# Performance work log

Hardware: AMD Instinct MI355X
Metric: run time of the kernel (lower is better)

## Reference

```python
import jax, jax.numpy as jnp
import numpy as np

N_NODES = 15
EMBED_DIM = 2048
F1 = 1024
F2 = 512
N_EDGES = 120


def gcn_conv(x, src, dst, W, b):
    # PyG GCNConv: h = D^{-1/2} (A + I) D^{-1/2} (x W) + b
    h = x @ W                                   # [N, F_out]
    n = h.shape[0]
    loops = jnp.arange(n)
    s = jnp.concatenate([src, loops])
    d = jnp.concatenate([dst, loops])
    deg = jax.ops.segment_sum(jnp.ones_like(d, dtype=h.dtype), d, num_segments=n)
    dinv = jax.lax.rsqrt(deg)                   # deg >= 1 due to self loops
    norm = dinv[s] * dinv[d]                    # [E+N]
    out = jax.ops.segment_sum(h[s] * norm[:, None], d, num_segments=n)
    return out + b


def attention_pool(x, attW):
    # SimGNN-style attention: global ctx = tanh(mean(x W)); scores = sigmoid(x @ ctx)
    ctx = jnp.tanh(jnp.mean(x @ attW, axis=0))  # [F2]
    scores = jax.nn.sigmoid(x @ ctx)            # [N]
    return x.T @ scores                         # [F2]


def setup_inputs() -> dict:
    key = jax.random.key(0)
    ks = jax.random.split(key, 16)
    d = {}
    d['features_1'] = jax.random.normal(ks[0], (N_NODES,), dtype=jnp.float32)
    d['edge_index_1'] = jax.random.randint(ks[1], (2, N_EDGES), 0, N_NODES, dtype=jnp.int32)
    d['target'] = jax.random.uniform(ks[2], (3,), dtype=jnp.float32)
    def lin(k, fi, fo):
        s = 1.0 / np.sqrt(fi)
        kw, kb = jax.random.split(k)
        return (jax.random.uniform(kw, (fi, fo), minval=-s, maxval=s, dtype=jnp.float32),
                jax.random.uniform(kb, (fo,), minval=-s, maxval=s, dtype=jnp.float32))
    d['W1'], d['b1'] = lin(ks[3], 15, 15 * 32)
    d['W2'], d['b2'] = lin(ks[4], 15 * 32, 15 * 128)
    d['W3'], d['b3'] = lin(ks[5], 15 * 128, 15 * EMBED_DIM)
    d['gW1'], d['gb1'] = lin(ks[6], EMBED_DIM, F1)
    d['gW2'], d['gb2'] = lin(ks[7], F1, F2)
    d['attW'] = jax.random.normal(ks[8], (F2, F2), dtype=jnp.float32) * (1.0 / np.sqrt(F2))
    d['fcW'], d['fcb'] = lin(ks[9], F2, 3)
    return d


def reference(features_1, edge_index_1, target, W1, b1, W2, b2, W3, b3,
              gW1, gb1, gW2, gb2, attW, fcW, fcb):
    # embed MLP: 15 -> 480 -> 1920 -> 15*embed_dim
    h = jax.nn.relu(features_1 @ W1 + b1)
    h = jax.nn.relu(h @ W2 + b2)
    h = (h @ W3 + b3).reshape(N_NODES, EMBED_DIM)
    src, dst = edge_index_1[0], edge_index_1[1]
    x = jax.nn.relu(gcn_conv(h, src, dst, gW1, gb1))
    x = gcn_conv(x, src, dst, gW2, gb2)
    rep = attention_pool(x, attW)               # [F2]
    logits = rep @ fcW + fcb                    # [3]
    cls = jnp.argmax(target)
    loss = -jax.nn.log_softmax(logits)[cls]
    predictions = jax.nn.softmax(logits)
    return loss, predictions
```

## Files before the change

kernel.cpp:

```cpp
#include <hip/hip_runtime.h>
#include <math.h>

#define NN 15
#define EMBED 2048
#define F1D 1024
#define F2D 512
#define NE 120
#define H1_DIM 480
#define H2_DIM 1920
#define H3_DIM 30720

#define OFF_A    0
#define OFF_H2   256
#define OFF_P3   2304
#define OFF_XG1  248064
#define OFF_P1   278784
#define OFF_XG2  524544
#define OFF_P2   539904
#define OFF_X2   662784
#define OFF_XBAR 670464
#define OFF_CTX  670976

__device__ inline void f4ma(float4& a, float s, const float4& w) {
    a.x += s * w.x; a.y += s * w.y; a.z += s * w.z; a.w += s * w.w;
}
__device__ inline void f4acc(float4& a, const float4& b) {
    a.x += b.x; a.y += b.y; a.z += b.z; a.w += b.w;
}

__global__ void k1_h2(const float* __restrict__ f, const float* __restrict__ W1,
                      const float* __restrict__ b1, const float* __restrict__ W2,
                      const float* __restrict__ b2, const int* __restrict__ edges,
                      float* __restrict__ ws) {
    int tid = threadIdx.x;
    if (blockIdx.x == 60) {
        __shared__ float dinv[NN];
        __shared__ float A[NN * NN];
        if (tid < NN) {
            int deg = 1;
            for (int i = 0; i < NE; ++i) deg += (edges[NE + i] == tid) ? 1 : 0;
            dinv[tid] = rsqrtf((float)deg);
        }
        __syncthreads();
        if (tid < NN * NN) {
            int r = tid / NN, c = tid % NN;
            A[tid] = (r == c) ? dinv[r] * dinv[r] : 0.0f;
        }
        __syncthreads();
        if (tid == 0) {
            for (int i = 0; i < NE; ++i) {
                int s = edges[i], d = edges[NE + i];
                A[d * NN + s] += dinv[s] * dinv[d];
            }
        }
        __syncthreads();
        if (tid < NN * NN) ws[OFF_A + tid] = A[tid];
        return;
    }
    __shared__ float h1[H1_DIM];
    __shared__ float4 red[32][8];
    float fr[NN];
#pragma unroll
    for (int k = 0; k < NN; ++k) fr[k] = f[k];
    for (int j = tid; j < H1_DIM; j += 256) {
        float acc = b1[j];
#pragma unroll
        for (int k = 0; k < NN; ++k) acc += fr[k] * W1[k * H1_DIM + j];
        h1[j] = fmaxf(acc, 0.0f);
    }
    __syncthreads();
    int jg = tid & 7, kc = tid >> 3;
    int j = blockIdx.x * 32 + jg * 4;
    float4 acc = make_float4(0.f, 0.f, 0.f, 0.f);
    for (int r = 0; r < 15; ++r) {
        int k = kc * 15 + r;
        float4 w = *(const float4*)(W2 + k * H2_DIM + j);
        f4ma(acc, h1[k], w);
    }
    red[kc][jg] = acc;
    __syncthreads();
    for (int s = 16; s >= 1; s >>= 1) {
        if (kc < s) f4acc(red[kc][jg], red[kc + s][jg]);
        __syncthreads();
    }
    if (kc == 0) {
        float4 b = *(const float4*)(b2 + j);
        float4 v = red[0][jg];
        v.x = fmaxf(v.x + b.x, 0.f); v.y = fmaxf(v.y + b.y, 0.f);
        v.z = fmaxf(v.z + b.z, 0.f); v.w = fmaxf(v.w + b.w, 0.f);
        *(float4*)(ws + OFF_H2 + j) = v;
    }
}

__global__ void k2_h3(const float* __restrict__ W3, float* __restrict__ ws) {
    __shared__ float h2l[240];
    __shared__ float4 red[128];
    int tid = threadIdx.x;
    int cb = blockIdx.x, kc = blockIdx.y;
    int kbase = kc * 240;
    for (int i = tid; i < 240; i += 256) h2l[i] = ws[OFF_H2 + kbase + i];
    __syncthreads();
    int f4i = tid & 127, rg = tid >> 7;
    int col = cb * 512 + f4i * 4;
    float4 acc = make_float4(0.f, 0.f, 0.f, 0.f);
    const float* wp = W3 + (size_t)(kbase + rg) * H3_DIM + col;
#pragma unroll 8
    for (int i = 0; i < 120; ++i) {
        float4 w = *(const float4*)wp;
        f4ma(acc, h2l[2 * i + rg], w);
        wp += 2 * (size_t)H3_DIM;
    }
    if (rg == 1) red[f4i] = acc;
    __syncthreads();
    if (rg == 0) {
        f4acc(acc, red[f4i]);
        *(float4*)(ws + OFF_P3 + (size_t)kc * H3_DIM + col) = acc;
    }
}

__global__ void k3_agg1(const float* __restrict__ b3, float* __restrict__ ws) {
    __shared__ float Al[NN * NN];
    __shared__ float S[NN][32];
    int tid = threadIdx.x;
    int c0 = blockIdx.x * 32;
    for (int i = tid; i < NN * NN; i += 256) Al[i] = ws[OFF_A + i];
    for (int q = tid; q < NN * 32; q += 256) {
        int m = q >> 5, c = q & 31;
        int j = m * EMBED + c0 + c;
        float s = b3[j];
#pragma unroll
        for (int p = 0; p < 8; ++p) s += ws[OFF_P3 + p * H3_DIM + j];
        S[m][c] = s;
    }
    __syncthreads();
    for (int q = tid; q < NN * 32; q += 256) {
        int n = q >> 5, c = q & 31;
        float x = 0.f;
#pragma unroll
        for (int m = 0; m < NN; ++m) x += Al[n * NN + m] * S[m][c];
        ws[OFF_XG1 + n * EMBED + c0 + c] = x;
    }
}

template<int IN, int OUT, int ECH>
__global__ void k_mmP(const float* __restrict__ X, const float* __restrict__ W,
                      float* __restrict__ P) {
    __shared__ float Xl[NN * ECH];
    __shared__ float4 red[8][32][NN];
    int tid = threadIdx.x;
    int e0 = blockIdx.y * ECH;
    for (int i = tid; i < NN * ECH; i += 256) {
        int n = i / ECH, e = i - n * ECH;
        Xl[i] = X[n * IN + e0 + e];
    }
    __syncthreads();
    int fg = tid & 31, kt = tid >> 5;
    int f = blockIdx.x * 128 + fg * 4;
    float4 acc[NN];
#pragma unroll
    for (int n = 0; n < NN; ++n) acc[n] = make_float4(0.f, 0.f, 0.f, 0.f);
    const int RPT = ECH / 8;
    for (int r = 0; r < RPT; ++r) {
        int e = kt * RPT + r;
        float4 w = *(const float4*)(W + (size_t)(e0 + e) * OUT + f);
#pragma unroll
        for (int n = 0; n < NN; ++n) f4ma(acc[n], Xl[n * ECH + e], w);
    }
    __syncthreads();
#pragma unroll
    for (int n = 0; n < NN; ++n) red[kt][fg][n] = acc[n];
    __syncthreads();
    for (int s = 4; s >= 1; s >>= 1) {
        if (kt < s) {
#pragma unroll
            for (int n = 0; n < NN; ++n) f4acc(red[kt][fg][n], red[kt + s][fg][n]);
        }
        __syncthreads();
    }
    if (kt == 0) {
#pragma unroll
        for (int n = 0; n < NN; ++n) {
            float4 v = red[0][fg][n];
            *(float4*)(P + (size_t)blockIdx.y * NN * OUT + n * OUT + f) = v;
        }
    }
}

__global__ void k5_fin1(const float* __restrict__ gb1, float* __restrict__ ws) {
    __shared__ float Al[NN * NN];
    __shared__ float S[NN][64];
    int tid = threadIdx.x;
    int f0 = blockIdx.x * 64;
    for (int i = tid; i < NN * NN; i += 256) Al[i] = ws[OFF_A + i];
    for (int q = tid; q < NN * 64; q += 256) {
        int n = q >> 6, c = q & 63;
        float s = gb1[f0 + c];
#pragma unroll
        for (int p = 0; p < 16; ++p) s += ws[OFF_P1 + p * (NN * F1D) + n * F1D + f0 + c];
        S[n][c] = fmaxf(s, 0.f);
    }
    __syncthreads();
    for (int q = tid; q < NN * 64; q += 256) {
        int n = q >> 6, c = q & 63;
        float x = 0.f;
#pragma unroll
        for (int m = 0; m < NN; ++m) x += Al[n * NN + m] * S[m][c];
        ws[OFF_XG2 + n * F1D + f0 + c] = x;
    }
}

__global__ void k7_fin2(const float* __restrict__ gb2, float* __restrict__ ws) {
    __shared__ float S[NN][64];
    int tid = threadIdx.x;
    int f0 = blockIdx.x * 64;
    for (int q = tid; q < NN * 64; q += 256) {
        int n = q >> 6, c = q & 63;
        float s = gb2[f0 + c];
#pragma unroll
        for (int p = 0; p < 16; ++p) s += ws[OFF_P2 + p * (NN * F2D) + n * F2D + f0 + c];
        S[n][c] = s;
        ws[OFF_X2 + n * F2D + f0 + c] = s;
    }
    __syncthreads();
    if (tid < 64) {
        float s = 0.f;
#pragma unroll
        for (int n = 0; n < NN; ++n) s += S[n][tid];
        ws[OFF_XBAR + f0 + tid] = s * (1.0f / 15.0f);
    }
}

__global__ void k8_ctx(const float* __restrict__ attW, float* __restrict__ ws) {
    __shared__ float xb[F2D];
    __shared__ float4 red[64][4];
    int tid = threadIdx.x;
    for (int e = tid; e < F2D; e += 256) xb[e] = ws[OFF_XBAR + e];
    __syncthreads();
    int fg = tid & 3, kt = tid >> 2;
    int f = blockIdx.x * 16 + fg * 4;
    float4 acc = make_float4(0.f, 0.f, 0.f, 0.f);
    for (int r = 0; r < 8; ++r) {
        int e = kt * 8 + r;
        float4 w = *(const float4*)(attW + e * F2D + f);
        f4ma(acc, xb[e], w);
    }
    red[kt][fg] = acc;
    __syncthreads();
    for (int s = 32; s >= 1; s >>= 1) {
        if (kt < s) f4acc(red[kt][fg], red[kt + s][fg]);
        __syncthreads();
    }
    if (kt == 0) {
        float4 v = red[0][fg];
        ws[OFF_CTX + f + 0] = tanhf(v.x);
        ws[OFF_CTX + f + 1] = tanhf(v.y);
        ws[OFF_CTX + f + 2] = tanhf(v.z);
        ws[OFF_CTX + f + 3] = tanhf(v.w);
    }
}

__global__ void k9_final(const float* __restrict__ fcW, const float* __restrict__ fcb,
                         const float* __restrict__ target, const float* __restrict__ ws,
                         float* __restrict__ out) {
    __shared__ float x2l[NN * F2D];
    __shared__ float ctxl[F2D];
    __shared__ float scores[16];
    __shared__ float rep[F2D];
    __shared__ float logits[3];
    int tid = threadIdx.x;
    for (int i = tid; i < NN * F2D; i += 256) x2l[i] = ws[OFF_X2 + i];
    for (int i = tid; i < F2D; i += 256) ctxl[i] = ws[OFF_CTX + i];
    __syncthreads();
    {
        int g = tid >> 4, l = tid & 15;
        if (g < NN) {
            float p = 0.f;
            for (int i = 0; i < 32; ++i) {
                int e = l + 16 * i;
                p += x2l[g * F2D + e] * ctxl[e];
            }
            p += __shfl_xor(p, 1); p += __shfl_xor(p, 2);
            p += __shfl_xor(p, 4); p += __shfl_xor(p, 8);
            if (l == 0) scores[g] = 1.0f / (1.0f + expf(-p));
        }
    }
    __syncthreads();
    for (int fi = tid; fi < F2D; fi += 256) {
        float v = 0.f;
#pragma unroll
        for (int n = 0; n < NN; ++n) v += x2l[n * F2D + fi] * scores[n];
        rep[fi] = v;
    }
    __syncthreads();
    if (tid < 192) {
        int j = tid >> 6, l = tid & 63;
        float p = 0.f;
        for (int i = 0; i < 8; ++i) {
            int e = l + 64 * i;
            p += rep[e] * fcW[e * 3 + j];
        }
        p += __shfl_xor(p, 1); p += __shfl_xor(p, 2); p += __shfl_xor(p, 4);
        p += __shfl_xor(p, 8); p += __shfl_xor(p, 16); p += __shfl_xor(p, 32);
        if (l == 0) logits[j] = p + fcb[j];
    }
    __syncthreads();
    if (tid == 0) {
        float t0 = target[0], t1 = target[1], t2 = target[2];
        int cls = 0; float best = t0;
        if (t1 > best) { best = t1; cls = 1; }
        if (t2 > best) { cls = 2; }
        float l0 = logits[0], l1 = logits[1], l2 = logits[2];
        float m = fmaxf(l0, fmaxf(l1, l2));
        float e0 = expf(l0 - m), e1 = expf(l1 - m), e2 = expf(l2 - m);
        float s = e0 + e1 + e2;
        float lc = (cls == 0) ? l0 : ((cls == 1) ? l1 : l2);
        out[0] = -(lc - m - logf(s));
        out[1] = e0 / s; out[2] = e1 / s; out[3] = e2 / s;
    }
}

extern "C" void kernel_launch(void* const* d_in, const int* in_sizes, int n_in,
                              void* d_out, int out_size, void* d_ws, size_t ws_size,
                              hipStream_t stream) {
    const float* f    = (const float*)d_in[0];
    const int*   ei   = (const int*)d_in[1];
    const float* tgt  = (const float*)d_in[2];
    const float* W1   = (const float*)d_in[3];
    const float* b1   = (const float*)d_in[4];
    const float* W2   = (const float*)d_in[5];
    const float* b2   = (const float*)d_in[6];
    const float* W3   = (const float*)d_in[7];
    const float* b3   = (const float*)d_in[8];
    const float* gW1  = (const float*)d_in[9];
    const float* gb1  = (const float*)d_in[10];
    const float* gW2  = (const float*)d_in[11];
    const float* gb2  = (const float*)d_in[12];
    const float* attW = (const float*)d_in[13];
    const float* fcW  = (const float*)d_in[14];
    const float* fcb  = (const float*)d_in[15];
    float* ws  = (float*)d_ws;
    float* out = (float*)d_out;

    k1_h2<<<dim3(61), dim3(256), 0, stream>>>(f, W1, b1, W2, b2, ei, ws);
    k2_h3<<<dim3(60, 8), dim3(256), 0, stream>>>(W3, ws);
    k3_agg1<<<dim3(64), dim3(256), 0, stream>>>(b3, ws);
    k_mmP<2048, 1024, 128><<<dim3(8, 16), dim3(256), 0, stream>>>(ws + OFF_XG1, gW1, ws + OFF_P1);
    k5_fin1<<<dim3(16), dim3(256), 0, stream>>>(gb1, ws);
    k_mmP<1024, 512, 64><<<dim3(4, 16), dim3(256), 0, stream>>>(ws + OFF_XG2, gW2, ws + OFF_P2);
    k7_fin2<<<dim3(8), dim3(256), 0, stream>>>(gb2, ws);
    k8_ctx<<<dim3(32), dim3(256), 0, stream>>>(attW, ws);
    k9_final<<<dim3(1), dim3(256), 0, stream>>>(fcW, fcb, tgt, ws, out);
}
```

Before: 414.2 us.

## Skip zero ReLU activations in W3 GEMV and reshape k2 grid

The h2 x W3 GEMV now compacts the nonzero post-ReLU h2 entries of each 120-row chunk into shared memory with a ballot and prefix popcount, then streams only those W3 rows. It uses nontemporal loads, and the grid changes to 32x16 blocks of 240 active threads covering 960 columns each. The reduction in k3 now sums 16 partials, and the workspace offsets are enlarged to hold them. Weight traffic scales with the number of nonzero activations, which ReLU typically makes about half, at the cost of an extra ballot step, a data-dependent loop trip count, and idle threads per block.

```diff
diff --git a/kernel.cpp b/kernel.cpp
--- a/kernel.cpp
+++ b/kernel.cpp
@@ -13,13 +13,15 @@
 #define OFF_A    0
 #define OFF_H2   256
 #define OFF_P3   2304
-#define OFF_XG1  248064
-#define OFF_P1   278784
-#define OFF_XG2  524544
-#define OFF_P2   539904
-#define OFF_X2   662784
-#define OFF_XBAR 670464
-#define OFF_CTX  670976
+#define OFF_XG1  493824
+#define OFF_P1   524544
+#define OFF_XG2  770304
+#define OFF_P2   785664
+#define OFF_X2   908544
+#define OFF_XBAR 916224
+#define OFF_CTX  916736
+
+typedef float vf4 __attribute__((ext_vector_type(4)));
 
 __device__ inline void f4ma(float4& a, float s, const float4& w) {
     a.x += s * w.x; a.y += s * w.y; a.z += s * w.z; a.w += s * w.w;
@@ -93,29 +95,37 @@
 }
 
 __global__ void k2_h3(const float* __restrict__ W3, float* __restrict__ ws) {
-    __shared__ float h2l[240];
-    __shared__ float4 red[128];
+    __shared__ float cval[120];
+    __shared__ int   coff[120];
+    __shared__ int   wcnt[2];
     int tid = threadIdx.x;
     int cb = blockIdx.x, kc = blockIdx.y;
-    int kbase = kc * 240;
-    for (int i = tid; i < 240; i += 256) h2l[i] = ws[OFF_H2 + kbase + i];
-    __syncthreads();
-    int f4i = tid & 127, rg = tid >> 7;
-    int col = cb * 512 + f4i * 4;
+    int kbase = kc * 120;
+    float hv = 0.0f;
+    if (tid < 120) hv = ws[OFF_H2 + kbase + tid];
+    int lane = tid & 63, wv = tid >> 6;
+    bool act = (tid < 120) && (hv != 0.0f);
+    unsigned long long m = __ballot(act);
+    if (wv < 2 && lane == 0) wcnt[wv] = __popcll(m);
+    __syncthreads();
+    if (act) {
+        int off = (wv == 1) ? wcnt[0] : 0;
+        int p = off + __popcll(m & ((1ull << lane) - 1ull));
+        coff[p] = (kbase + tid) * H3_DIM;
+        cval[p] = hv;
+    }
+    __syncthreads();
+    int nr = wcnt[0] + wcnt[1];
+    if (tid >= 240) return;
+    int col = cb * 960 + tid * 4;
     float4 acc = make_float4(0.f, 0.f, 0.f, 0.f);
-    const float* wp = W3 + (size_t)(kbase + rg) * H3_DIM + col;
 #pragma unroll 8
-    for (int i = 0; i < 120; ++i) {
-        float4 w = *(const float4*)wp;
-        f4ma(acc, h2l[2 * i + rg], w);
-        wp += 2 * (size_t)H3_DIM;
-    }
-    if (rg == 1) red[f4i] = acc;
-    __syncthreads();
-    if (rg == 0) {
-        f4acc(acc, red[f4i]);
-        *(float4*)(ws + OFF_P3 + (size_t)kc * H3_DIM + col) = acc;
-    }
+    for (int r = 0; r < nr; ++r) {
+        vf4 w = __builtin_nontemporal_load((const vf4*)(W3 + (size_t)coff[r] + col));
+        float s = cval[r];
+        acc.x += s * w.x; acc.y += s * w.y; acc.z += s * w.z; acc.w += s * w.w;
+    }
+    *(float4*)(ws + OFF_P3 + (size_t)kc * H3_DIM + col) = acc;
 }
 
 __global__ void k3_agg1(const float* __restrict__ b3, float* __restrict__ ws) {
@@ -129,7 +139,7 @@
         int j = m * EMBED + c0 + c;
         float s = b3[j];
 #pragma unroll
-        for (int p = 0; p < 8; ++p) s += ws[OFF_P3 + p * H3_DIM + j];
+        for (int p = 0; p < 16; ++p) s += ws[OFF_P3 + p * H3_DIM + j];
         S[m][c] = s;
     }
     __syncthreads();
@@ -342,7 +352,7 @@
     float* out = (float*)d_out;
 
     k1_h2<<<dim3(61), dim3(256), 0, stream>>>(f, W1, b1, W2, b2, ei, ws);
-    k2_h3<<<dim3(60, 8), dim3(256), 0, stream>>>(W3, ws);
+    k2_h3<<<dim3(32, 16), dim3(256), 0, stream>>>(W3, ws);
     k3_agg1<<<dim3(64), dim3(256), 0, stream>>>(b3, ws);
     k_mmP<2048, 1024, 128><<<dim3(8, 16), dim3(256), 0, stream>>>(ws + OFF_XG1, gW1, ws + OFF_P1);
     k5_fin1<<<dim3(16), dim3(256), 0, stream>>>(gb1, ws);
```

Measured after the change: 375.2 us (median of 2 runs). 9.4% less time.
